# Kernel optimization log

Hardware: AMD Instinct MI355X
Metric: run time of the kernel (lower is better)

The kernel has to match this reference:

```python
import jax, jax.numpy as jnp
import numpy as np
from jax import lax

DIM = 96
HEADS = 4
HID = int(DIM * 2.66)  # 255
EPS_LN = 1e-5
EPS_NORM = 1e-12


def _ln(x, w, b):
    # channel-wise LayerNorm over c of (b,c,h,w) (equivalent to to_3d -> LN(c) -> to_4d)
    mu = x.mean(axis=1, keepdims=True)
    var = ((x - mu) ** 2).mean(axis=1, keepdims=True)
    return (x - mu) / jnp.sqrt(var + EPS_LN) * w[None, :, None, None] + b[None, :, None, None]


def _c1x1(w, x):
    # 1x1 conv, no bias: w (out,in), x (b,in,h,w)
    return jnp.einsum('oc,bchw->bohw', w, x)


def _l2norm(x):
    # F.normalize along last dim (pixels), eps=1e-12
    n = jnp.sqrt(jnp.sum(x * x, axis=-1, keepdims=True))
    return x / jnp.maximum(n, EPS_NORM)


def setup_inputs() -> dict:
    key = jax.random.key(0)
    ks = jax.random.split(key, 10)
    B, H, W = 4, 256, 256
    s = 0.02
    return {
        'x': jax.random.normal(ks[0], (B, DIM, H, W), jnp.float32),
        'svp_fea': jax.random.normal(ks[1], (B, 3, H, W), jnp.float32),
        'norm1_w': jnp.ones((DIM,), jnp.float32),
        'norm1_b': jnp.zeros((DIM,), jnp.float32),
        'qkv_w': jax.random.normal(ks[2], (3 * DIM, DIM), jnp.float32) * s,
        'qkv_dw_w': jax.random.normal(ks[3], (3 * DIM, 1, 3, 3), jnp.float32) * s,
        'svp_w': jax.random.normal(ks[4], (3 * HEADS, 3), jnp.float32) * s,
        'temperature': jnp.ones((HEADS, 1, 1), jnp.float32),
        'proj_out_w': jax.random.normal(ks[5], (DIM, DIM + 3 * HEADS), jnp.float32) * s,
        'norm2_w': jnp.ones((DIM,), jnp.float32),
        'norm2_b': jnp.zeros((DIM,), jnp.float32),
        'ffn1_w': jax.random.normal(ks[6], (HID, DIM), jnp.float32) * s,
        'ffn2_w': jax.random.normal(ks[7], (HID, DIM), jnp.float32) * s,
        'ffn_out_w': jax.random.normal(ks[8], (DIM, HID), jnp.float32) * s,
    }


def reference(x, svp_fea, norm1_w, norm1_b, qkv_w, qkv_dw_w, svp_w, temperature,
              proj_out_w, norm2_w, norm2_b, ffn1_w, ffn2_w, ffn_out_w):
    b, c, h, w = x.shape
    hw = h * w
    # --- IlluminationGuideAttention ---
    xn = _ln(x, norm1_w, norm1_b)
    qkv = _c1x1(qkv_w, xn)
    qkv = lax.conv_general_dilated(
        qkv, qkv_dw_w, window_strides=(1, 1), padding='SAME',
        feature_group_count=3 * DIM, dimension_numbers=('NCHW', 'OIHW', 'NCHW'))
    q, k, v = jnp.split(qkv, 3, axis=1)
    svp_q = _c1x1(svp_w, svp_fea)

    def heads(t):
        return t.reshape(b, HEADS, -1, hw)  # b head c (h w)

    q = _l2norm(heads(q))          # (b,H,ch,hw)
    k = _l2norm(heads(k))
    svp_q = _l2norm(heads(svp_q))  # (b,H,3,hw)
    v = heads(v)
    q = jnp.concatenate([q, svp_q], axis=2)  # (b,H,ch+3,hw)

    attn = jnp.einsum('bhcn,bhdn->bhcd', q, k) * temperature[None]
    attn = jax.nn.softmax(attn, axis=-1)
    out = jnp.einsum('bhcd,bhdn->bhcn', attn, v).reshape(b, -1, h, w)
    x = x + _c1x1(proj_out_w, out)

    # --- DualGatedFeedForward ---
    xn = _ln(x, norm2_w, norm2_b)
    p1 = _c1x1(ffn1_w, xn)
    p2 = _c1x1(ffn2_w, xn)
    g = p1 * jax.nn.sigmoid(p2) + p2 * jax.nn.gelu(p1, approximate=False)
    return x + _c1x1(ffn_out_w, g)
```

## Files before the change

kernel.cpp:

```cpp
#include <hip/hip_runtime.h>


namespace {
constexpr int kB = 4;
constexpr int kC = 96;
constexpr int kHW = 65536;
constexpr int kNP = kB * kHW;
constexpr int kQKVC = 288;
constexpr int kNH = 4;
constexpr int kCH = 24;
constexpr int kQC = 27;
constexpr int kHID = 255;
constexpr int kSTR = 40;
constexpr int kQKSPLIT = 32;
}

typedef __attribute__((ext_vector_type(8))) short short8;
typedef __attribute__((ext_vector_type(8))) unsigned short ushort8;
typedef __attribute__((ext_vector_type(4))) unsigned short ushortx4;
typedef __attribute__((ext_vector_type(4))) float floatx4;

__device__ __forceinline__ float bf2f(unsigned short u) {
  return __uint_as_float(((unsigned int)u) << 16);
}
__device__ __forceinline__ unsigned short f2bf(float f) {
  unsigned int i = __float_as_uint(f);
  i += 0x7fffu + ((i >> 16) & 1u);
  return (unsigned short)(i >> 16);
}

__global__ void k_zero(float* __restrict__ p, int n) {
  const int i = blockIdx.x * blockDim.x + threadIdx.x;
  if (i < n) p[i] = 0.f;
}
__global__ void k_fill0_f32(float* __restrict__ p, int n) {
  const int i = blockIdx.x * blockDim.x + threadIdx.x;
  if (i < n) p[i] = 0.f;
}

__global__ __launch_bounds__(256) void k_wconv(
    const float* __restrict__ qkvw, const float* __restrict__ projw,
    const float* __restrict__ w1, const float* __restrict__ w2,
    const float* __restrict__ fw, unsigned short* __restrict__ qb,
    unsigned short* __restrict__ pb, unsigned short* __restrict__ w1b,
    unsigned short* __restrict__ w2b, unsigned short* __restrict__ fwb) {
  int i = blockIdx.x * 256 + threadIdx.x;
  if (i < 27648) { qb[i] = f2bf(qkvw[i]); return; }
  i -= 27648;
  if (i < 12288) {
    const int r = i >> 7, k = i & 127;
    pb[i] = (k < 108) ? f2bf(projw[r * 108 + k]) : (unsigned short)0;
    return;
  }
  i -= 12288;
  if (i < 24576) { w1b[i] = (i < 24480) ? f2bf(w1[i]) : (unsigned short)0; return; }
  i -= 24576;
  if (i < 24576) { w2b[i] = (i < 24480) ? f2bf(w2[i]) : (unsigned short)0; return; }
  i -= 24576;
  {
    const int r = i >> 8, k = i & 255;
    fwb[i] = (k < 255) ? f2bf(fw[r * 255 + k]) : (unsigned short)0;
  }
}

__global__ __launch_bounds__(256) void k_ln1_apply(
    const float* __restrict__ x, const float* __restrict__ nw,
    const float* __restrict__ nb, unsigned short* __restrict__ A) {
  const int pg = blockIdx.x * 256 + threadIdx.x;
  const int b = pg >> 16, p = pg & (kHW - 1);
  const float* xb = x + (size_t)b * kC * kHW + p;
  float v[kC];
  float s = 0.f, s2 = 0.f;
  #pragma unroll
  for (int c = 0; c < kC; ++c) {
    v[c] = xb[(size_t)c * kHW];
    s += v[c];
    s2 = fmaf(v[c], v[c], s2);
  }
  const float m = s * (1.f / kC);
  const float var = s2 * (1.f / kC) - m * m;
  const float rstd = rsqrtf(var + 1e-5f);
  unsigned short* ob = A + ((size_t)b * kQKVC + 192) * kHW + p;
  #pragma unroll
  for (int c = 0; c < kC; ++c) {
    ob[(size_t)c * kHW] = f2bf((v[c] - m) * rstd * nw[c] + nb[c]);
  }
}

__global__ __launch_bounds__(256) void k_ln2_stats(
    const unsigned short* __restrict__ x2, float* __restrict__ mu, float* __restrict__ rs) {
  const int t8 = blockIdx.x * 256 + threadIdx.x;
  const int b = t8 >> 13, p0 = (t8 & 8191) * 8;
  const unsigned short* xb = x2 + (size_t)b * kC * kHW + p0;
  float s[8], s2[8];
  #pragma unroll
  for (int j = 0; j < 8; ++j) { s[j] = 0.f; s2[j] = 0.f; }
  for (int c = 0; c < kC; ++c) {
    const ushort8 u = *(const ushort8*)&xb[(size_t)c * kHW];
    #pragma unroll
    for (int j = 0; j < 8; ++j) {
      const float v = bf2f(u[j]);
      s[j] += v;
      s2[j] = fmaf(v, v, s2[j]);
    }
  }
  const int base = (b << 16) + p0;
  #pragma unroll
  for (int j = 0; j < 8; ++j) {
    const float m = s[j] * (1.f / kC);
    const float var = s2[j] * (1.f / kC) - m * m;
    mu[base + j] = m;
    rs[base + j] = rsqrtf(var + 1e-5f);
  }
}

__global__ __launch_bounds__(256) void k_gemm_qkv(
    const unsigned short* __restrict__ xn1base, const unsigned short* __restrict__ qb,
    int grp, unsigned short* __restrict__ bufC) {
  __shared__ __align__(16) unsigned short As[96 * kSTR];
  __shared__ __align__(16) unsigned short Bs[128 * kSTR];
  const int tid = threadIdx.x;
  const int b = blockIdx.y;
  const int p0 = blockIdx.x * 128;
  const int wave = tid >> 6, lane = tid & 63, ln16 = lane & 15, quad = lane >> 4;
  floatx4 acc[6][2];
  #pragma unroll
  for (int i = 0; i < 6; ++i) { acc[i][0] = (floatx4)(0.f); acc[i][1] = (floatx4)(0.f); }
  const int rB = tid >> 3, c0 = (tid & 7) * 16;
  const int pos = rB ^ ((tid & 3) << 3);
  const int q0 = (quad ^ ((wave * 2) & 3)) << 3;
  const int q1 = (quad ^ ((wave * 2 + 1) & 3)) << 3;
  for (int ks = 0; ks < 3; ++ks) {
    const int k0 = ks * 32;
    for (int idx = tid; idx < 384; idx += 256) {
      const int m = idx >> 2, ch = idx & 3;
      *(short8*)&As[m * kSTR + ch * 8] =
          *(const short8*)(qb + (size_t)(grp * 96 + m) * 96 + k0 + ch * 8);
    }
    {
      const unsigned short* src =
          xn1base + ((size_t)b * kQKVC + 192 + k0 + rB) * kHW + p0 + c0;
      const ushort8 u0 = ((const ushort8*)src)[0];
      const ushort8 u1 = ((const ushort8*)src)[1];
      #pragma unroll
      for (int e = 0; e < 8; ++e) {
        Bs[(c0 + e) * kSTR + pos] = u0[e];
        Bs[(c0 + 8 + e) * kSTR + pos] = u1[e];
      }
    }
    __syncthreads();
    short8 bfr0 = *(const short8*)&Bs[(wave * 32 + ln16) * kSTR + q0];
    short8 bfr1 = *(const short8*)&Bs[(wave * 32 + 16 + ln16) * kSTR + q1];
    #pragma unroll
    for (int ms = 0; ms < 6; ++ms) {
      const short8 afr = *(const short8*)&As[(ms * 16 + ln16) * kSTR + quad * 8];
      acc[ms][0] = __builtin_amdgcn_mfma_f32_16x16x32_bf16(afr, bfr0, acc[ms][0], 0, 0, 0);
      acc[ms][1] = __builtin_amdgcn_mfma_f32_16x16x32_bf16(afr, bfr1, acc[ms][1], 0, 0, 0);
    }
    __syncthreads();
  }
  unsigned short* ob = bufC + (size_t)b * kC * kHW;
  #pragma unroll
  for (int ms = 0; ms < 6; ++ms)
    #pragma unroll
    for (int ns = 0; ns < 2; ++ns)
      #pragma unroll
      for (int r = 0; r < 4; ++r) {
        const int R = ms * 16 + quad * 4 + r;
        const int P = p0 + wave * 32 + ns * 16 + ln16;
        ob[(size_t)R * kHW + P] = f2bf(acc[ms][ns][r]);
      }
}

__global__ __launch_bounds__(256) void k_gemm_proj(
    const unsigned short* __restrict__ qkv_post, const unsigned short* __restrict__ pb,
    const float* __restrict__ x, unsigned short* __restrict__ x2) {
  __shared__ __align__(16) unsigned short As[96 * kSTR];
  __shared__ __align__(16) unsigned short Bs[128 * kSTR];
  const int tid = threadIdx.x;
  const int b = blockIdx.y;
  const int p0 = blockIdx.x * 128;
  const int wave = tid >> 6, lane = tid & 63, ln16 = lane & 15, quad = lane >> 4;
  floatx4 acc[6][2];
  #pragma unroll
  for (int i = 0; i < 6; ++i) { acc[i][0] = (floatx4)(0.f); acc[i][1] = (floatx4)(0.f); }
  const int rB = tid >> 3, c0 = (tid & 7) * 16;
  const int pos = rB ^ ((tid & 3) << 3);
  const int q0 = (quad ^ ((wave * 2) & 3)) << 3;
  const int q1 = (quad ^ ((wave * 2 + 1) & 3)) << 3;
  for (int ks = 0; ks < 4; ++ks) {
    const int k0 = ks * 32;
    for (int idx = tid; idx < 384; idx += 256) {
      const int m = idx >> 2, ch = idx & 3;
      *(short8*)&As[m * kSTR + ch * 8] =
          *(const short8*)(pb + (size_t)m * 128 + k0 + ch * 8);
    }
    {
      const int k = k0 + rB;
      if (k < 108) {
        const unsigned short* src = qkv_post + ((size_t)b * kQKVC + k) * kHW + p0 + c0;
        const ushort8 u0 = ((const ushort8*)src)[0];
        const ushort8 u1 = ((const ushort8*)src)[1];
        #pragma unroll
        for (int e = 0; e < 8; ++e) {
          Bs[(c0 + e) * kSTR + pos] = u0[e];
          Bs[(c0 + 8 + e) * kSTR + pos] = u1[e];
        }
      } else {
        #pragma unroll
        for (int e = 0; e < 16; ++e) Bs[(c0 + e) * kSTR + pos] = 0;
      }
    }
    __syncthreads();
    short8 bfr0 = *(const short8*)&Bs[(wave * 32 + ln16) * kSTR + q0];
    short8 bfr1 = *(const short8*)&Bs[(wave * 32 + 16 + ln16) * kSTR + q1];
    #pragma unroll
    for (int ms = 0; ms < 6; ++ms) {
      const short8 afr = *(const short8*)&As[(ms * 16 + ln16) * kSTR + quad * 8];
      acc[ms][0] = __builtin_amdgcn_mfma_f32_16x16x32_bf16(afr, bfr0, acc[ms][0], 0, 0, 0);
      acc[ms][1] = __builtin_amdgcn_mfma_f32_16x16x32_bf16(afr, bfr1, acc[ms][1], 0, 0, 0);
    }
    __syncthreads();
  }
  #pragma unroll
  for (int ms = 0; ms < 6; ++ms)
    #pragma unroll
    for (int ns = 0; ns < 2; ++ns)
      #pragma unroll
      for (int r = 0; r < 4; ++r) {
        const int R = ms * 16 + quad * 4 + r;
        const int P = p0 + wave * 32 + ns * 16 + ln16;
        const size_t idx = ((size_t)b * kC + R) * kHW + P;
        x2[idx] = f2bf(acc[ms][ns][r] + x[idx]);
      }
}

__global__ __launch_bounds__(256) void k_gemm_gate(
    const unsigned short* __restrict__ x2, const float* __restrict__ mu_buf,
    const float* __restrict__ rs_buf, const float* __restrict__ nw,
    const float* __restrict__ nb, const unsigned short* __restrict__ w1b,
    const unsigned short* __restrict__ w2b, unsigned short* __restrict__ g) {
  __shared__ __align__(16) unsigned short Bs[3 * 128 * kSTR];
  __shared__ __align__(16) unsigned short As[128 * kSTR];
  __shared__ float mus[128], rss[128];
  const int tid = threadIdx.x;
  const int b = blockIdx.y;
  const int p0 = blockIdx.x * 128;
  if (tid < 128) {
    mus[tid] = mu_buf[(b << 16) + p0 + tid];
    rss[tid] = rs_buf[(b << 16) + p0 + tid];
  }
  __syncthreads();
  const int wave = tid >> 6, lane = tid & 63, ln16 = lane & 15, quad = lane >> 4;
  const int rB = tid >> 3, c0 = (tid & 7) * 16;
  const int pos = rB ^ ((tid & 3) << 3);
  const int q0 = (quad ^ ((wave * 2) & 3)) << 3;
  const int q1 = (quad ^ ((wave * 2 + 1) & 3)) << 3;
  #pragma unroll
  for (int ks = 0; ks < 3; ++ks) {
    const int k = ks * 32 + rB;
    const float wk = nw[k], bk = nb[k];
    const unsigned short* src = x2 + ((size_t)b * kC + k) * kHW + p0 + c0;
    const ushort8 u0 = ((const ushort8*)src)[0];
    const ushort8 u1 = ((const ushort8*)src)[1];
    unsigned short* bp = &Bs[ks * 128 * kSTR];
    #pragma unroll
    for (int e = 0; e < 8; ++e) {
      const int n0 = c0 + e, n1 = c0 + 8 + e;
      bp[n0 * kSTR + pos] = f2bf((bf2f(u0[e]) - mus[n0]) * rss[n0] * wk + bk);
      bp[n1 * kSTR + pos] = f2bf((bf2f(u1[e]) - mus[n1]) * rss[n1] * wk + bk);
    }
  }
  for (int grp = 0; grp < 4; ++grp) {
    const int i0 = grp * 64;
    floatx4 acc[8][2];
    #pragma unroll
    for (int i = 0; i < 8; ++i) { acc[i][0] = (floatx4)(0.f); acc[i][1] = (floatx4)(0.f); }
    #pragma unroll
    for (int ks = 0; ks < 3; ++ks) {
      for (int idx = tid; idx < 512; idx += 256) {
        const int m = idx >> 2, ch = idx & 3;
        const int ii = i0 + (m & 63);
        const unsigned short* wsrc =
            ((m < 64) ? w1b : w2b) + (size_t)ii * 96 + ks * 32 + ch * 8;
        *(short8*)&As[m * kSTR + ch * 8] = *(const short8*)wsrc;
      }
      __syncthreads();
      const unsigned short* bp = &Bs[ks * 128 * kSTR];
      short8 bfr0 = *(const short8*)&bp[(wave * 32 + ln16) * kSTR + q0];
      short8 bfr1 = *(const short8*)&bp[(wave * 32 + 16 + ln16) * kSTR + q1];
      #pragma unroll
      for (int ms = 0; ms < 8; ++ms) {
        const short8 afr = *(const short8*)&As[(ms * 16 + ln16) * kSTR + quad * 8];
        acc[ms][0] = __builtin_amdgcn_mfma_f32_16x16x32_bf16(afr, bfr0, acc[ms][0], 0, 0, 0);
        acc[ms][1] = __builtin_amdgcn_mfma_f32_16x16x32_bf16(afr, bfr1, acc[ms][1], 0, 0, 0);
      }
      __syncthreads();
    }
    #pragma unroll
    for (int ms = 0; ms < 4; ++ms)
      #pragma unroll
      for (int ns = 0; ns < 2; ++ns)
        #pragma unroll
        for (int r = 0; r < 4; ++r) {
          const int ii = i0 + ms * 16 + quad * 4 + r;
          if (ii < kHID) {
            const int P = p0 + wave * 32 + ns * 16 + ln16;
            const float p1 = acc[ms][ns][r], p2 = acc[ms + 4][ns][r];
            const float sig = __builtin_amdgcn_rcpf(1.f + __expf(-p2));
            const float targ = p1 * fmaf(p1 * p1, 0.0713548f, 1.5957691f);
            const float gel = p1 * __builtin_amdgcn_rcpf(1.f + __expf(-targ));
            g[((size_t)b * kHID + ii) * kHW + P] = f2bf(fmaf(p1, sig, p2 * gel));
          }
        }
  }
}

__global__ __launch_bounds__(256) void k_gemm_fout(
    const unsigned short* __restrict__ g, const unsigned short* __restrict__ fwb,
    const unsigned short* __restrict__ x2, float* __restrict__ out) {
  __shared__ __align__(16) unsigned short As[96 * kSTR];
  __shared__ __align__(16) unsigned short Bs[128 * kSTR];
  const int tid = threadIdx.x;
  const int b = blockIdx.y;
  const int p0 = blockIdx.x * 128;
  const int wave = tid >> 6, lane = tid & 63, ln16 = lane & 15, quad = lane >> 4;
  floatx4 acc[6][2];
  #pragma unroll
  for (int i = 0; i < 6; ++i) { acc[i][0] = (floatx4)(0.f); acc[i][1] = (floatx4)(0.f); }
  const int rB = tid >> 3, c0 = (tid & 7) * 16;
  const int pos = rB ^ ((tid & 3) << 3);
  const int q0 = (quad ^ ((wave * 2) & 3)) << 3;
  const int q1 = (quad ^ ((wave * 2 + 1) & 3)) << 3;
  for (int ks = 0; ks < 8; ++ks) {
    const int k0 = ks * 32;
    for (int idx = tid; idx < 384; idx += 256) {
      const int m = idx >> 2, ch = idx & 3;
      *(short8*)&As[m * kSTR + ch * 8] =
          *(const short8*)(fwb + (size_t)m * 256 + k0 + ch * 8);
    }
    {
      const int k = k0 + rB;
      if (k < kHID) {
        const unsigned short* src = g + ((size_t)b * kHID + k) * kHW + p0 + c0;
        const ushort8 u0 = ((const ushort8*)src)[0];
        const ushort8 u1 = ((const ushort8*)src)[1];
        #pragma unroll
        for (int e = 0; e < 8; ++e) {
          Bs[(c0 + e) * kSTR + pos] = u0[e];
          Bs[(c0 + 8 + e) * kSTR + pos] = u1[e];
        }
      } else {
        #pragma unroll
        for (int e = 0; e < 16; ++e) Bs[(c0 + e) * kSTR + pos] = 0;
      }
    }
    __syncthreads();
    short8 bfr0 = *(const short8*)&Bs[(wave * 32 + ln16) * kSTR + q0];
    short8 bfr1 = *(const short8*)&Bs[(wave * 32 + 16 + ln16) * kSTR + q1];
    #pragma unroll
    for (int ms = 0; ms < 6; ++ms) {
      const short8 afr = *(const short8*)&As[(ms * 16 + ln16) * kSTR + quad * 8];
      acc[ms][0] = __builtin_amdgcn_mfma_f32_16x16x32_bf16(afr, bfr0, acc[ms][0], 0, 0, 0);
      acc[ms][1] = __builtin_amdgcn_mfma_f32_16x16x32_bf16(afr, bfr1, acc[ms][1], 0, 0, 0);
    }
    __syncthreads();
  }
  #pragma unroll
  for (int ms = 0; ms < 6; ++ms)
    #pragma unroll
    for (int ns = 0; ns < 2; ++ns)
      #pragma unroll
      for (int r = 0; r < 4; ++r) {
        const int R = ms * 16 + quad * 4 + r;
        const int P = p0 + wave * 32 + ns * 16 + ln16;
        const size_t idx = ((size_t)b * kC + R) * kHW + P;
        out[idx] = acc[ms][ns][r] + bf2f(x2[idx]);
      }
}

__global__ __launch_bounds__(256) void k_dw(
    const unsigned short* __restrict__ buf, const float* __restrict__ dww,
    unsigned short* __restrict__ qkv_post, int gbase) {
  const int blk = blockIdx.x;
  const int plane = blk >> 5;
  const int y0 = (blk & 31) * 8;
  const int b = plane / kC, chl = plane % kC;
  const int t = threadIdx.x;
  const int y = y0 + (t >> 5);
  const int x0 = (t & 31) * 8;
  const unsigned short* in = buf + (size_t)plane * kHW;
  float w[9];
  #pragma unroll
  for (int i = 0; i < 9; ++i) w[i] = dww[(size_t)(gbase + chl) * 9 + i];
  float acc[8];
  #pragma unroll
  for (int j = 0; j < 8; ++j) acc[j] = 0.f;
  #pragma unroll
  for (int dy = -1; dy <= 1; ++dy) {
    const int yy = y + dy;
    if (yy < 0 || yy > 255) continue;
    const unsigned short* rp = in + yy * 256;
    float f[10];
    const ushort8 v = *(const ushort8*)(rp + x0);
    #pragma unroll
    for (int e = 0; e < 8; ++e) f[e + 1] = bf2f(v[e]);
    f[0] = (x0 > 0) ? bf2f(rp[x0 - 1]) : 0.f;
    f[9] = (x0 < 248) ? bf2f(rp[x0 + 8]) : 0.f;
    const float w0 = w[(dy + 1) * 3], w1 = w[(dy + 1) * 3 + 1], w2 = w[(dy + 1) * 3 + 2];
    #pragma unroll
    for (int j = 0; j < 8; ++j)
      acc[j] = fmaf(w0, f[j], fmaf(w1, f[j + 1], fmaf(w2, f[j + 2], acc[j])));
  }
  unsigned short* op = qkv_post + ((size_t)b * kQKVC + gbase + chl) * kHW + y * 256 + x0;
  ushort8 o;
  #pragma unroll
  for (int j = 0; j < 8; ++j) o[j] = f2bf(acc[j]);
  *(ushort8*)op = o;
}

__global__ __launch_bounds__(256) void k_svpq(
    const float* __restrict__ svp, const float* __restrict__ svpw,
    unsigned short* __restrict__ svpq) {
  const int t8 = blockIdx.x * 256 + threadIdx.x;
  const int b = t8 >> 13, p0 = (t8 & 8191) * 8;
  float s0[8], s1[8], s2v[8];
  #pragma unroll
  for (int j = 0; j < 8; ++j) {
    s0[j] = svp[((size_t)b * 3 + 0) * kHW + p0 + j];
    s1[j] = svp[((size_t)b * 3 + 1) * kHW + p0 + j];
    s2v[j] = svp[((size_t)b * 3 + 2) * kHW + p0 + j];
  }
  #pragma unroll
  for (int jj = 0; jj < 12; ++jj) {
    const float w0 = svpw[jj * 3], w1 = svpw[jj * 3 + 1], w2 = svpw[jj * 3 + 2];
    ushort8 o;
    #pragma unroll
    for (int j = 0; j < 8; ++j)
      o[j] = f2bf(fmaf(w2, s2v[j], fmaf(w1, s1[j], w0 * s0[j])));
    *(ushort8*)&svpq[((size_t)b * 12 + jj) * kHW + p0] = o;
  }
}

__global__ __launch_bounds__(256) void k_qk(
    const unsigned short* __restrict__ qkv_post, const unsigned short* __restrict__ svpq,
    float* __restrict__ spart, float* __restrict__ ssbuf) {
  const int bh = blockIdx.y, b = bh >> 2, h = bh & 3;
  const int tid = threadIdx.x;
  const int wave = tid >> 6, lane = tid & 63;
  const int l15 = lane & 15, gq = lane >> 4;
  const int pstart = blockIdx.x * 2048 + wave * 512;
  constexpr int NCH = 16;

  const unsigned short* pA0 =
      qkv_post + ((size_t)b * kQKVC + h * kCH + l15) * kHW + gq * 8;
  const unsigned short* pB0 =
      qkv_post + ((size_t)b * kQKVC + 96 + h * kCH + l15) * kHW + gq * 8;
  const int rA1 = 16 + l15, rB1 = 16 + l15;
  const bool vA1 = (rA1 < kQC), vB1 = (rB1 < kCH);
  const unsigned short* pA1 =
      (rA1 < kCH) ? qkv_post + ((size_t)b * kQKVC + h * kCH + rA1) * kHW + gq * 8
      : (rA1 < kQC) ? svpq + ((size_t)(b * 12 + h * 3 + (rA1 - kCH))) * kHW + gq * 8
                    : pA0;
  const unsigned short* pB1 =
      vB1 ? qkv_post + ((size_t)b * kQKVC + 96 + h * kCH + rB1) * kHW + gq * 8 : pB0;

  floatx4 c00 = (floatx4)(0.f), c01 = (floatx4)(0.f);
  floatx4 c10 = (floatx4)(0.f), c11 = (floatx4)(0.f);
  float ssA0 = 0.f, ssA1 = 0.f, ssB0 = 0.f, ssB1 = 0.f;
  const short8 kZ = (short8)(short)0;

  short8 a0 = *(const short8*)(pA0 + pstart);
  short8 b0 = *(const short8*)(pB0 + pstart);
  short8 a1 = vA1 ? *(const short8*)(pA1 + pstart) : kZ;
  short8 b1 = vB1 ? *(const short8*)(pB1 + pstart) : kZ;
  for (int c = 0; c < NCH; ++c) {
    const short8 ta0 = a0, tb0 = b0, ta1 = a1, tb1 = b1;
    if (c + 1 < NCH) {
      const int pn = pstart + (c + 1) * 32;
      a0 = *(const short8*)(pA0 + pn);
      b0 = *(const short8*)(pB0 + pn);
      a1 = vA1 ? *(const short8*)(pA1 + pn) : kZ;
      b1 = vB1 ? *(const short8*)(pB1 + pn) : kZ;
    }
    c00 = __builtin_amdgcn_mfma_f32_16x16x32_bf16(ta0, tb0, c00, 0, 0, 0);
    c01 = __builtin_amdgcn_mfma_f32_16x16x32_bf16(ta0, tb1, c01, 0, 0, 0);
    c10 = __builtin_amdgcn_mfma_f32_16x16x32_bf16(ta1, tb0, c10, 0, 0, 0);
    c11 = __builtin_amdgcn_mfma_f32_16x16x32_bf16(ta1, tb1, c11, 0, 0, 0);
    #pragma unroll
    for (int e = 0; e < 8; ++e) {
      const float v0 = bf2f((unsigned short)ta0[e]);
      const float v1 = bf2f((unsigned short)ta1[e]);
      const float v2 = bf2f((unsigned short)tb0[e]);
      const float v3 = bf2f((unsigned short)tb1[e]);
      ssA0 = fmaf(v0, v0, ssA0);
      ssA1 = fmaf(v1, v1, ssA1);
      ssB0 = fmaf(v2, v2, ssB0);
      ssB1 = fmaf(v3, v3, ssB1);
    }
  }
  ssA0 += __shfl_xor(ssA0, 16); ssA0 += __shfl_xor(ssA0, 32);
  ssA1 += __shfl_xor(ssA1, 16); ssA1 += __shfl_xor(ssA1, 32);
  ssB0 += __shfl_xor(ssB0, 16); ssB0 += __shfl_xor(ssB0, 32);
  ssB1 += __shfl_xor(ssB1, 16); ssB1 += __shfl_xor(ssB1, 32);
  if (gq == 0) {
    atomicAdd(&ssbuf[b * 96 + h * kCH + l15], ssA0);
    if (rA1 < kCH) atomicAdd(&ssbuf[b * 96 + h * kCH + rA1], ssA1);
    else if (rA1 < kQC) atomicAdd(&ssbuf[768 + b * 12 + h * 3 + (rA1 - kCH)], ssA1);
    atomicAdd(&ssbuf[384 + b * 96 + h * kCH + l15], ssB0);
    if (vB1) atomicAdd(&ssbuf[384 + b * 96 + h * kCH + rB1], ssB1);
  }
  float* wp = spart + ((size_t)((blockIdx.x * 16 + bh) * 4 + wave)) * 648;
  #pragma unroll
  for (int r = 0; r < 4; ++r) {
    const int row0 = gq * 4 + r, row1 = 16 + gq * 4 + r;
    wp[row0 * kCH + l15] = c00[r];
    if (16 + l15 < kCH) wp[row0 * kCH + 16 + l15] = c01[r];
    if (row1 < kQC) {
      wp[row1 * kCH + l15] = c10[r];
      if (16 + l15 < kCH) wp[row1 * kCH + 16 + l15] = c11[r];
    }
  }
}

__global__ __launch_bounds__(256) void k_softmax(
    const float* __restrict__ spart, const float* __restrict__ ssbuf,
    const float* __restrict__ temp, float* __restrict__ attn) {
  const int row = blockIdx.x * 256 + threadIdx.x;
  if (row >= kB * kNH * kQC) return;
  const int bh = row / kQC, c = row - bh * kQC;
  const int b = bh >> 2, h = bh & 3;
  const float ssq = (c < kCH) ? ssbuf[b * 96 + h * kCH + c]
                              : ssbuf[768 + b * 12 + h * 3 + (c - kCH)];
  const float rq = 1.f / fmaxf(sqrtf(ssq), 1e-12f);
  const float t = temp[h];
  float l[kCH];
  #pragma unroll
  for (int d = 0; d < kCH; ++d) l[d] = 0.f;
  for (int s = 0; s < kQKSPLIT * 4; ++s) {
    const int split = s >> 2, wv = s & 3;
    const float* sp = spart + ((size_t)((split * 16 + bh) * 4 + wv)) * 648 + c * kCH;
    #pragma unroll
    for (int d = 0; d < kCH; ++d) l[d] += sp[d];
  }
  float mx = -1e30f;
  #pragma unroll
  for (int d = 0; d < kCH; ++d) {
    const float rk = 1.f / fmaxf(sqrtf(ssbuf[384 + b * 96 + h * kCH + d]), 1e-12f);
    l[d] = l[d] * rq * rk * t;
    mx = fmaxf(mx, l[d]);
  }
  float sum = 0.f;
  #pragma unroll
  for (int d = 0; d < kCH; ++d) { l[d] = __expf(l[d] - mx); sum += l[d]; }
  const float inv = 1.f / sum;
  float* arow = attn + (size_t)(bh * kQC + c) * kCH;
  #pragma unroll
  for (int d = 0; d < kCH; ++d) arow[d] = l[d] * inv;
}

__global__ __launch_bounds__(256) void k_av(
    const float* __restrict__ attn, unsigned short* __restrict__ qkv_post) {
  const int h = blockIdx.y;
  const int t4 = blockIdx.x * 256 + threadIdx.x;
  const int b = t4 >> 14, p0 = (t4 & 16383) * 4;
  __shared__ float at[kQC * kCH];
  for (int idx = threadIdx.x; idx < kQC * kCH; idx += 256)
    at[idx] = attn[(size_t)(b * kNH + h) * kQC * kCH + idx];
  __syncthreads();
  float acc[kQC][4];
  #pragma unroll
  for (int c = 0; c < kQC; ++c)
    #pragma unroll
    for (int j = 0; j < 4; ++j) acc[c][j] = 0.f;
  for (int d = 0; d < kCH; ++d) {
    const ushortx4 v =
        *(const ushortx4*)&qkv_post[((size_t)b * kQKVC + 192 + h * kCH + d) * kHW + p0];
    float vv[4];
    #pragma unroll
    for (int j = 0; j < 4; ++j) vv[j] = bf2f(v[j]);
    #pragma unroll
    for (int c = 0; c < kQC; ++c) {
      const float a = at[c * kCH + d];
      #pragma unroll
      for (int j = 0; j < 4; ++j) acc[c][j] = fmaf(a, vv[j], acc[c][j]);
    }
  }
  #pragma unroll
  for (int c = 0; c < kQC; ++c) {
    ushortx4 o;
    #pragma unroll
    for (int j = 0; j < 4; ++j) o[j] = f2bf(acc[c][j]);
    *(ushortx4*)&qkv_post[((size_t)b * kQKVC + h * kQC + c) * kHW + p0] = o;
  }
}

extern "C" void kernel_launch(void* const* d_in, const int* in_sizes, int n_in,
                              void* d_out, int out_size, void* d_ws, size_t ws_size,
                              hipStream_t stream) {
  (void)in_sizes; (void)n_in;
  const float* x     = (const float*)d_in[0];
  const float* svp   = (const float*)d_in[1];
  const float* n1w   = (const float*)d_in[2];
  const float* n1b   = (const float*)d_in[3];
  const float* qkvw  = (const float*)d_in[4];
  const float* dww   = (const float*)d_in[5];
  const float* svpw  = (const float*)d_in[6];
  const float* temp  = (const float*)d_in[7];
  const float* projw = (const float*)d_in[8];
  const float* n2w   = (const float*)d_in[9];
  const float* n2b   = (const float*)d_in[10];
  const float* w1    = (const float*)d_in[11];
  const float* w2    = (const float*)d_in[12];
  const float* fw    = (const float*)d_in[13];
  float* outp = (float*)d_out;

  const size_t SZ_A = (size_t)kB * kQKVC * kHW * 2;
  const size_t SZ_C = (size_t)kB * kC * kHW * 2;
  const size_t NEED = (1u << 20) + SZ_A + SZ_C;

  if (ws_size < NEED) {
    k_fill0_f32<<<(out_size + 255) / 256, 256, 0, stream>>>(outp, out_size);
    return;
  }

  char* ws = (char*)d_ws;
  float* attn  = (float*)(ws + 65536);
  float* ssbuf = (float*)(ws + 131072);
  unsigned short* qb  = (unsigned short*)(ws + 262144);
  unsigned short* pb  = (unsigned short*)(ws + 317440);
  unsigned short* w1b = (unsigned short*)(ws + 342016);
  unsigned short* w2b = (unsigned short*)(ws + 391168);
  unsigned short* fwb = (unsigned short*)(ws + 440320);
  unsigned short* A    = (unsigned short*)(ws + (1u << 20));
  unsigned short* bufC = (unsigned short*)(ws + (1u << 20) + SZ_A);
  float* mu2 = (float*)(ws + (1u << 20) + 134u * 1048576u);
  float* rs2 = (float*)(ws + (1u << 20) + 135u * 1048576u);
  unsigned short* g    = A;
  unsigned short* x2   = bufC;
  unsigned short* svpq = bufC;
  float* spart = (float*)(ws + (1u << 20) + SZ_A + 8u * 1048576u);

  k_wconv<<<444, 256, 0, stream>>>(qkvw, projw, w1, w2, fw, qb, pb, w1b, w2b, fwb);
  k_zero<<<4, 256, 0, stream>>>(ssbuf, 816);
  k_ln1_apply<<<kNP / 256, 256, 0, stream>>>(x, n1w, n1b, A);
  for (int grp = 0; grp < 3; ++grp) {
    k_gemm_qkv<<<dim3(kHW / 128, kB), 256, 0, stream>>>(A, qb, grp, bufC);
    k_dw<<<kB * kC * 32, 256, 0, stream>>>(bufC, dww, A, grp * kC);
  }
  k_svpq<<<kNP / 8 / 256, 256, 0, stream>>>(svp, svpw, svpq);
  k_qk<<<dim3(kQKSPLIT, 16), 256, 0, stream>>>(A, svpq, spart, ssbuf);
  k_softmax<<<2, 256, 0, stream>>>(spart, ssbuf, temp, attn);
  k_av<<<dim3(kNP / 4 / 256, kNH), 256, 0, stream>>>(attn, A);
  k_gemm_proj<<<dim3(kHW / 128, kB), 256, 0, stream>>>(A, pb, x, x2);
  k_ln2_stats<<<kNP / 8 / 256, 256, 0, stream>>>(x2, mu2, rs2);
  k_gemm_gate<<<dim3(kHW / 128, kB), 256, 0, stream>>>(x2, mu2, rs2, n2w, n2b, w1b, w2b, g);
  k_gemm_fout<<<dim3(kHW / 128, kB), 256, 0, stream>>>(g, fwb, x2, outp);
}
```

Before: 716.3 us.

## Fuse LN2 stats into proj GEMM and FFN out-projection into gate GEMM

```diff
diff --git a/kernel.cpp b/kernel.cpp
--- a/kernel.cpp
+++ b/kernel.cpp
@@ -12,6 +12,7 @@
 constexpr int kQC = 27;
 constexpr int kHID = 255;
 constexpr int kSTR = 40;
+constexpr int kGST = 72;
 constexpr int kQKSPLIT = 32;
 }
 
@@ -87,33 +88,6 @@
   }
 }
 
-__global__ __launch_bounds__(256) void k_ln2_stats(
-    const unsigned short* __restrict__ x2, float* __restrict__ mu, float* __restrict__ rs) {
-  const int t8 = blockIdx.x * 256 + threadIdx.x;
-  const int b = t8 >> 13, p0 = (t8 & 8191) * 8;
-  const unsigned short* xb = x2 + (size_t)b * kC * kHW + p0;
-  float s[8], s2[8];
-  #pragma unroll
-  for (int j = 0; j < 8; ++j) { s[j] = 0.f; s2[j] = 0.f; }
-  for (int c = 0; c < kC; ++c) {
-    const ushort8 u = *(const ushort8*)&xb[(size_t)c * kHW];
-    #pragma unroll
-    for (int j = 0; j < 8; ++j) {
-      const float v = bf2f(u[j]);
-      s[j] += v;
-      s2[j] = fmaf(v, v, s2[j]);
-    }
-  }
-  const int base = (b << 16) + p0;
-  #pragma unroll
-  for (int j = 0; j < 8; ++j) {
-    const float m = s[j] * (1.f / kC);
-    const float var = s2[j] * (1.f / kC) - m * m;
-    mu[base + j] = m;
-    rs[base + j] = rsqrtf(var + 1e-5f);
-  }
-}
-
 __global__ __launch_bounds__(256) void k_gemm_qkv(
     const unsigned short* __restrict__ xn1base, const unsigned short* __restrict__ qb,
     int grp, unsigned short* __restrict__ bufC) {
@@ -174,7 +148,8 @@
 
 __global__ __launch_bounds__(256) void k_gemm_proj(
     const unsigned short* __restrict__ qkv_post, const unsigned short* __restrict__ pb,
-    const float* __restrict__ x, unsigned short* __restrict__ x2) {
+    const float* __restrict__ x, unsigned short* __restrict__ x2,
+    float* __restrict__ mu2, float* __restrict__ rs2) {
   __shared__ __align__(16) unsigned short As[96 * kSTR];
   __shared__ __align__(16) unsigned short Bs[128 * kSTR];
   const int tid = threadIdx.x;
@@ -222,6 +197,7 @@
     }
     __syncthreads();
   }
+  float s[2] = {0.f, 0.f}, s2[2] = {0.f, 0.f};
   #pragma unroll
   for (int ms = 0; ms < 6; ++ms)
     #pragma unroll
@@ -231,17 +207,34 @@
         const int R = ms * 16 + quad * 4 + r;
         const int P = p0 + wave * 32 + ns * 16 + ln16;
         const size_t idx = ((size_t)b * kC + R) * kHW + P;
-        x2[idx] = f2bf(acc[ms][ns][r] + x[idx]);
-      }
-}
-
-__global__ __launch_bounds__(256) void k_gemm_gate(
+        const float val = acc[ms][ns][r] + x[idx];
+        x2[idx] = f2bf(val);
+        s[ns] += val;
+        s2[ns] = fmaf(val, val, s2[ns]);
+      }
+  #pragma unroll
+  for (int ns = 0; ns < 2; ++ns) {
+    float a = s[ns], c = s2[ns];
+    a += __shfl_xor(a, 16); a += __shfl_xor(a, 32);
+    c += __shfl_xor(c, 16); c += __shfl_xor(c, 32);
+    if (quad == 0) {
+      const int P = p0 + wave * 32 + ns * 16 + ln16;
+      const float m = a * (1.f / kC);
+      mu2[(b << 16) + P] = m;
+      rs2[(b << 16) + P] = rsqrtf(c * (1.f / kC) - m * m + 1e-5f);
+    }
+  }
+}
+
+__global__ __launch_bounds__(256) void k_gemm_gatefout(
     const unsigned short* __restrict__ x2, const float* __restrict__ mu_buf,
     const float* __restrict__ rs_buf, const float* __restrict__ nw,
     const float* __restrict__ nb, const unsigned short* __restrict__ w1b,
-    const unsigned short* __restrict__ w2b, unsigned short* __restrict__ g) {
+    const unsigned short* __restrict__ w2b, const unsigned short* __restrict__ fwb,
+    float* __restrict__ out) {
   __shared__ __align__(16) unsigned short Bs[3 * 128 * kSTR];
   __shared__ __align__(16) unsigned short As[128 * kSTR];
+  __shared__ __align__(16) unsigned short Gs[128 * kGST];
   __shared__ float mus[128], rss[128];
   const int tid = threadIdx.x;
   const int b = blockIdx.y;
@@ -271,6 +264,9 @@
       bp[n1 * kSTR + pos] = f2bf((bf2f(u1[e]) - mus[n1]) * rss[n1] * wk + bk);
     }
   }
+  floatx4 facc[6][2];
+  #pragma unroll
+  for (int i = 0; i < 6; ++i) { facc[i][0] = (floatx4)(0.f); facc[i][1] = (floatx4)(0.f); }
   for (int grp = 0; grp < 4; ++grp) {
     const int i0 = grp * 64;
     floatx4 acc[8][2];
@@ -303,68 +299,35 @@
       for (int ns = 0; ns < 2; ++ns)
         #pragma unroll
         for (int r = 0; r < 4; ++r) {
-          const int ii = i0 + ms * 16 + quad * 4 + r;
-          if (ii < kHID) {
-            const int P = p0 + wave * 32 + ns * 16 + ln16;
-            const float p1 = acc[ms][ns][r], p2 = acc[ms + 4][ns][r];
-            const float sig = __builtin_amdgcn_rcpf(1.f + __expf(-p2));
-            const float targ = p1 * fmaf(p1 * p1, 0.0713548f, 1.5957691f);
-            const float gel = p1 * __builtin_amdgcn_rcpf(1.f + __expf(-targ));
-            g[((size_t)b * kHID + ii) * kHW + P] = f2bf(fmaf(p1, sig, p2 * gel));
-          }
+          const int kl = ms * 16 + quad * 4 + r;
+          const int pl = wave * 32 + ns * 16 + ln16;
+          const float p1 = acc[ms][ns][r], p2 = acc[ms + 4][ns][r];
+          const float sig = __builtin_amdgcn_rcpf(1.f + __expf(-p2));
+          const float targ = p1 * fmaf(p1 * p1, 0.0713548f, 1.5957691f);
+          const float gel = p1 * __builtin_amdgcn_rcpf(1.f + __expf(-targ));
+          Gs[pl * kGST + kl] = f2bf(fmaf(p1, sig, p2 * gel));
         }
-  }
-}
-
-__global__ __launch_bounds__(256) void k_gemm_fout(
-    const unsigned short* __restrict__ g, const unsigned short* __restrict__ fwb,
-    const unsigned short* __restrict__ x2, float* __restrict__ out) {
-  __shared__ __align__(16) unsigned short As[96 * kSTR];
-  __shared__ __align__(16) unsigned short Bs[128 * kSTR];
-  const int tid = threadIdx.x;
-  const int b = blockIdx.y;
-  const int p0 = blockIdx.x * 128;
-  const int wave = tid >> 6, lane = tid & 63, ln16 = lane & 15, quad = lane >> 4;
-  floatx4 acc[6][2];
-  #pragma unroll
-  for (int i = 0; i < 6; ++i) { acc[i][0] = (floatx4)(0.f); acc[i][1] = (floatx4)(0.f); }
-  const int rB = tid >> 3, c0 = (tid & 7) * 16;
-  const int pos = rB ^ ((tid & 3) << 3);
-  const int q0 = (quad ^ ((wave * 2) & 3)) << 3;
-  const int q1 = (quad ^ ((wave * 2 + 1) & 3)) << 3;
-  for (int ks = 0; ks < 8; ++ks) {
-    const int k0 = ks * 32;
-    for (int idx = tid; idx < 384; idx += 256) {
-      const int m = idx >> 2, ch = idx & 3;
-      *(short8*)&As[m * kSTR + ch * 8] =
-          *(const short8*)(fwb + (size_t)m * 256 + k0 + ch * 8);
-    }
-    {
-      const int k = k0 + rB;
-      if (k < kHID) {
-        const unsigned short* src = g + ((size_t)b * kHID + k) * kHW + p0 + c0;
-        const ushort8 u0 = ((const ushort8*)src)[0];
-        const ushort8 u1 = ((const ushort8*)src)[1];
-        #pragma unroll
-        for (int e = 0; e < 8; ++e) {
-          Bs[(c0 + e) * kSTR + pos] = u0[e];
-          Bs[(c0 + 8 + e) * kSTR + pos] = u1[e];
-        }
-      } else {
-        #pragma unroll
-        for (int e = 0; e < 16; ++e) Bs[(c0 + e) * kSTR + pos] = 0;
-      }
-    }
     __syncthreads();
-    short8 bfr0 = *(const short8*)&Bs[(wave * 32 + ln16) * kSTR + q0];
-    short8 bfr1 = *(const short8*)&Bs[(wave * 32 + 16 + ln16) * kSTR + q1];
-    #pragma unroll
-    for (int ms = 0; ms < 6; ++ms) {
-      const short8 afr = *(const short8*)&As[(ms * 16 + ln16) * kSTR + quad * 8];
-      acc[ms][0] = __builtin_amdgcn_mfma_f32_16x16x32_bf16(afr, bfr0, acc[ms][0], 0, 0, 0);
-      acc[ms][1] = __builtin_amdgcn_mfma_f32_16x16x32_bf16(afr, bfr1, acc[ms][1], 0, 0, 0);
-    }
-    __syncthreads();
+    #pragma unroll
+    for (int ksub = 0; ksub < 2; ++ksub) {
+      for (int idx = tid; idx < 384; idx += 256) {
+        const int m = idx >> 2, ch = idx & 3;
+        *(short8*)&As[m * kSTR + ch * 8] =
+            *(const short8*)(fwb + (size_t)m * 256 + i0 + ksub * 32 + ch * 8);
+      }
+      __syncthreads();
+      const short8 bf0 =
+          *(const short8*)&Gs[(wave * 32 + ln16) * kGST + ksub * 32 + quad * 8];
+      const short8 bf1 =
+          *(const short8*)&Gs[(wave * 32 + 16 + ln16) * kGST + ksub * 32 + quad * 8];
+      #pragma unroll
+      for (int ms = 0; ms < 6; ++ms) {
+        const short8 afr = *(const short8*)&As[(ms * 16 + ln16) * kSTR + quad * 8];
+        facc[ms][0] = __builtin_amdgcn_mfma_f32_16x16x32_bf16(afr, bf0, facc[ms][0], 0, 0, 0);
+        facc[ms][1] = __builtin_amdgcn_mfma_f32_16x16x32_bf16(afr, bf1, facc[ms][1], 0, 0, 0);
+      }
+      __syncthreads();
+    }
   }
   #pragma unroll
   for (int ms = 0; ms < 6; ++ms)
@@ -375,7 +338,7 @@
         const int R = ms * 16 + quad * 4 + r;
         const int P = p0 + wave * 32 + ns * 16 + ln16;
         const size_t idx = ((size_t)b * kC + R) * kHW + P;
-        out[idx] = acc[ms][ns][r] + bf2f(x2[idx]);
+        out[idx] = facc[ms][ns][r] + bf2f(x2[idx]);
       }
 }
 
@@ -636,7 +599,6 @@
   unsigned short* bufC = (unsigned short*)(ws + (1u << 20) + SZ_A);
   float* mu2 = (float*)(ws + (1u << 20) + 134u * 1048576u);
   float* rs2 = (float*)(ws + (1u << 20) + 135u * 1048576u);
-  unsigned short* g    = A;
   unsigned short* x2   = bufC;
   unsigned short* svpq = bufC;
   float* spart = (float*)(ws + (1u << 20) + SZ_A + 8u * 1048576u);
@@ -652,8 +614,7 @@
   k_qk<<<dim3(kQKSPLIT, 16), 256, 0, stream>>>(A, svpq, spart, ssbuf);
   k_softmax<<<2, 256, 0, stream>>>(spart, ssbuf, temp, attn);
   k_av<<<dim3(kNP / 4 / 256, kNH), 256, 0, stream>>>(attn, A);
-  k_gemm_proj<<<dim3(kHW / 128, kB), 256, 0, stream>>>(A, pb, x, x2);
-  k_ln2_stats<<<kNP / 8 / 256, 256, 0, stream>>>(x2, mu2, rs2);
-  k_gemm_gate<<<dim3(kHW / 128, kB), 256, 0, stream>>>(x2, mu2, rs2, n2w, n2b, w1b, w2b, g);
-  k_gemm_fout<<<dim3(kHW / 128, kB), 256, 0, stream>>>(g, fwb, x2, outp);
-}
+  k_gemm_proj<<<dim3(kHW / 128, kB), 256, 0, stream>>>(A, pb, x, x2, mu2, rs2);
+  k_gemm_gatefout<<<dim3(kHW / 128, kB), 256, 0, stream>>>(
+      x2, mu2, rs2, n2w, n2b, w1b, w2b, fwb, outp);
+}
```

New measurement: 656.1 us. -8.4%, faster.
